# Kernel tuning notes

Measured on AMD Instinct MI355X. Metric: run time of the kernel, lower is better.

Reference implementation:

```python
import jax, jax.numpy as jnp
import numpy as np

H = 16          # query heads
KV = 8          # kv heads
D = 256         # head_dim
HID = 3584      # hidden_size
ROPE_BASE = 10000.0
SCALING = 256.0 ** -0.5          # query_pre_attn_scalar ** -0.5
SOFTCAP = 50.0                   # attn_logit_softcapping
WINDOW = 1536 - 1                # sliding_window - 1 (layer_idx 0 is even)


def _rope_neox(x, positions):
    # x: [T, nh, D]; neox style: rotate the two halves of the head dim
    half = D // 2
    inv_freq = 1.0 / (ROPE_BASE ** (jnp.arange(0, D, 2, dtype=jnp.float32) / D))  # [half]
    freqs = positions.astype(jnp.float32)[:, None] * inv_freq[None, :]            # [T, half]
    cos = jnp.cos(freqs)[:, None, :]  # [T, 1, half]
    sin = jnp.sin(freqs)[:, None, :]
    x1, x2 = x[..., :half], x[..., half:]
    return jnp.concatenate([x1 * cos - x2 * sin, x2 * cos + x1 * sin], axis=-1)


def setup_inputs() -> dict:
    key = jax.random.key(0)
    k1, k2, k3 = jax.random.split(key, 3)
    T = 3072
    hidden_states = jax.random.normal(k1, (T, HID), dtype=jnp.float32)
    w_qkv = jax.random.normal(k2, (H * D + 2 * KV * D, HID), dtype=jnp.float32) * 0.02
    w_o = jax.random.normal(k3, (HID, H * D), dtype=jnp.float32) * 0.02
    positions = jnp.arange(T, dtype=jnp.int64)
    return {"positions": positions, "hidden_states": hidden_states,
            "w_qkv": w_qkv, "w_o": w_o}


def reference(positions, hidden_states, w_qkv, w_o):
    T = hidden_states.shape[0]
    qkv = hidden_states @ w_qkv.T                       # [T, (H+2KV)*D]
    q, k, v = jnp.split(qkv, [H * D, H * D + KV * D], axis=-1)
    q = q.reshape(T, H, D)
    k = k.reshape(T, KV, D)
    v = v.reshape(T, KV, D)
    q = _rope_neox(q, positions)
    k = _rope_neox(k, positions)
    # GQA: repeat kv heads (2 query heads per kv head)
    k = jnp.repeat(k, H // KV, axis=1)                  # [T, H, D]
    v = jnp.repeat(v, H // KV, axis=1)
    scores = jnp.einsum('thd,shd->hts', q, k) * SCALING  # [H, T, T]
    scores = SOFTCAP * jnp.tanh(scores / SOFTCAP)       # logit softcapping
    i = positions[:, None]
    j = positions[None, :]
    mask = (j <= i) & (i - j <= WINDOW)                 # causal + sliding window
    scores = jnp.where(mask[None, :, :], scores, -jnp.inf)
    probs = jax.nn.softmax(scores, axis=-1)
    attn = jnp.einsum('hts,shd->thd', probs, v).reshape(T, H * D)
    return attn @ w_o.T                                 # [T, HID]
```

## Files before the change

kernel.cpp:

```cpp
#include <hip/hip_runtime.h>
#include <math.h>

typedef unsigned short u16;
typedef __attribute__((ext_vector_type(8))) short short8;
typedef __attribute__((ext_vector_type(4))) float f32x4;
typedef __attribute__((ext_vector_type(4))) unsigned short u16x4;

#define HN 16
#define KVH 8
#define DH 256
#define HID 3584
#define T_LEN 3072
#define QKV_N 8192
#define O_N 4096
#define WIN 1535
#define SCALING 0.0625f
#define SOFTCAP 50.0f
#define KOFF 4096
#define VOFF 6144
#define PSTR 72
#define NJT 48
#define M_FIX 20.0f

__device__ __forceinline__ u16 f2bf(float f) {
  unsigned u = __float_as_uint(f);
  u += 0x7FFFu + ((u >> 16) & 1u);
  return (u16)(u >> 16);
}
__device__ __forceinline__ float bf2f(u16 b) {
  return __uint_as_float(((unsigned)b) << 16);
}

__device__ __forceinline__ void gload_lds16(const void* g, void* l) {
  __builtin_amdgcn_global_load_lds(
      (const __attribute__((address_space(1))) void*)g,
      (__attribute__((address_space(3))) void*)l, 16, 0, 0);
}

__device__ __forceinline__ f32x4 mfma_bf16(short8 a, short8 b, f32x4 c) {
  return __builtin_amdgcn_mfma_f32_16x16x32_bf16(a, b, c, 0, 0, 0);
}

#define BARX()                                  \
  do {                                          \
    __builtin_amdgcn_sched_barrier(0);          \
    __builtin_amdgcn_s_barrier();               \
    __builtin_amdgcn_sched_barrier(0);          \
  } while (0)

__global__ __launch_bounds__(256) void cvt2_kernel(const float* __restrict__ a,
                                                   u16* __restrict__ da, int nva,
                                                   const float* __restrict__ b,
                                                   u16* __restrict__ db, int nvb,
                                                   float* __restrict__ rtab) {
  const int bid = blockIdx.x;
  if (bid < 1536) {
    int idx = bid * 256 + threadIdx.x;
    int d = idx & 127;
    int t = idx >> 7;
    float inv = exp2f((float)d * (-13.287712379549449f / 128.0f));
    float ang = (float)t * inv;
    float2 cs;
    cs.x = cosf(ang);
    cs.y = sinf(ang);
    *(float2*)(rtab + (size_t)idx * 2) = cs;
  }
  int v = bid * 256 + threadIdx.x;
  const float* src;
  u16* dst;
  if (v < nva) {
    src = a + (size_t)v * 4;
    dst = da + (size_t)v * 4;
  } else if (v < nva + nvb) {
    int u = v - nva;
    src = b + (size_t)u * 4;
    dst = db + (size_t)u * 4;
  } else {
    return;
  }
  float4 x = *(const float4*)src;
  u16x4 o;
  o[0] = f2bf(x.x); o[1] = f2bf(x.y); o[2] = f2bf(x.z); o[3] = f2bf(x.w);
  *(u16x4*)dst = o;
}

template <int OUT_BF16, int ROPE>
__global__ __launch_bounds__(512, 2) void gemm8p(const u16* __restrict__ A,
                                                 const u16* __restrict__ B,
                                                 void* __restrict__ Cv,
                                                 int N, int K, int ntn, int cpx,
                                                 const float* __restrict__ rtab) {
  __shared__ u16 sA[2][256 * 64];
  __shared__ u16 sB[2][256 * 64];

  const int bid = blockIdx.x;
  const int tid = threadIdx.x;
  const int wg = (bid & 7) * cpx + (bid >> 3);
  const int bm = wg / ntn, bn = wg % ntn;
  const int row0 = bm * 256, col0 = bn * 256;
  const int lane = tid & 63, wid = tid >> 6;
  const int wr = wid >> 2, wc = wid & 3;
  const int NT = K >> 6;

  const int srow = lane >> 3;
  const int sg = (lane & 7) ^ srow;

  auto stage = [&](int tau, int kind) {
    if (tau >= NT) return;
    const int b = tau & 1;
    const int rbase = (kind & 1) * 128;
    const u16* src;
    u16* dst;
    if (kind >= 2) {
      src = A + (size_t)(row0 + rbase + wid * 8 + srow) * K + (size_t)tau * 64 + sg * 8;
      dst = &sA[b][(rbase + wid * 8) * 64];
    } else {
      src = B + (size_t)(col0 + rbase + wid * 8 + srow) * K + (size_t)tau * 64 + sg * 8;
      dst = &sB[b][(rbase + wid * 8) * 64];
    }
    gload_lds16(src, dst);
    gload_lds16(src + (size_t)64 * K, dst + 64 * 64);
  };

  f32x4 acc[8][4] = {};
  const int fr = lane & 15;
  const int fh = fr & 7;
  const int gk0 = (lane >> 4) ^ fh;
  const int gk1 = ((lane >> 4) + 4) ^ fh;

  stage(0, 0); stage(0, 1); stage(0, 2); stage(0, 3);
  stage(1, 0); stage(1, 1); stage(1, 2);
  __builtin_amdgcn_sched_barrier(0);
  asm volatile("s_waitcnt vmcnt(6)" ::: "memory");
  BARX();

  for (int u = 0; u < NT; ++u) {
    const int b = u & 1;
    const u16* pA = &sA[b][0];
    const u16* pB = &sB[b][0];
    short8 bf[4][2], afA[2][2], afB[2][2];

#define CMAP(ni) (wc * 32 + ((ni) & 1) * 16 + ((ni) >> 1) * 128)
#define LDB_(ni, kk) (*(const short8*)&pB[(CMAP(ni) + fr) * 64 + (kk ? gk1 : gk0) * 8])
#define LDA_(mi, kk) (*(const short8*)&pA[(wr * 128 + (mi)*16 + fr) * 64 + (kk ? gk1 : gk0) * 8])
#define MFMA2(AF, mi0)                                                   \
  __builtin_amdgcn_s_setprio(1);                                        \
  _Pragma("unroll") for (int ni = 0; ni < 4; ++ni) {                    \
    acc[mi0][ni] = mfma_bf16(AF[0][0], bf[ni][0], acc[mi0][ni]);        \
    acc[mi0][ni] = mfma_bf16(AF[0][1], bf[ni][1], acc[mi0][ni]);        \
    acc[mi0 + 1][ni] = mfma_bf16(AF[1][0], bf[ni][0], acc[mi0 + 1][ni]);\
    acc[mi0 + 1][ni] = mfma_bf16(AF[1][1], bf[ni][1], acc[mi0 + 1][ni]);\
  }                                                                      \
  __builtin_amdgcn_s_setprio(0);                                        \
  asm volatile("s_waitcnt lgkmcnt(0)" ::: "memory");

#pragma unroll
    for (int ni = 0; ni < 4; ++ni) { bf[ni][0] = LDB_(ni, 0); bf[ni][1] = LDB_(ni, 1); }
    afA[0][0] = LDA_(0, 0); afA[0][1] = LDA_(0, 1);
    afA[1][0] = LDA_(1, 0); afA[1][1] = LDA_(1, 1);
    stage(u + 1, 3);
    BARX();
    MFMA2(afA, 0);
    BARX();
    afA[0][0] = LDA_(2, 0); afA[0][1] = LDA_(2, 1);
    afA[1][0] = LDA_(3, 0); afA[1][1] = LDA_(3, 1);
    stage(u + 2, 0);
    BARX();
    MFMA2(afA, 2);
    BARX();
    afA[0][0] = LDA_(4, 0); afA[0][1] = LDA_(4, 1);
    afA[1][0] = LDA_(5, 0); afA[1][1] = LDA_(5, 1);
    afB[0][0] = LDA_(6, 0); afB[0][1] = LDA_(6, 1);
    afB[1][0] = LDA_(7, 0); afB[1][1] = LDA_(7, 1);
    stage(u + 2, 1);
    BARX();
    MFMA2(afA, 4);
    BARX();
    stage(u + 2, 2);
    __builtin_amdgcn_sched_barrier(0);
    if (u + 2 < NT) {
      asm volatile("s_waitcnt vmcnt(6)" ::: "memory");
    } else {
      asm volatile("s_waitcnt vmcnt(0)" ::: "memory");
    }
    BARX();
    MFMA2(afB, 6);
    BARX();
#undef LDB_
#undef LDA_
#undef MFMA2
  }

  if (ROPE && bn < 24) {
#pragma unroll
    for (int mi = 0; mi < 8; ++mi) {
#pragma unroll
      for (int nh = 0; nh < 2; ++nh) {
        const int dlo = wc * 32 + nh * 16 + fr;
#pragma unroll
        for (int j = 0; j < 4; ++j) {
          const int r = row0 + wr * 128 + mi * 16 + (lane >> 4) * 4 + j;
          float2 cs = *(const float2*)(rtab + ((size_t)(r << 7) + dlo) * 2);
          float xlo = acc[mi][nh][j];
          float xhi = acc[mi][nh + 2][j];
          ((u16*)Cv)[(size_t)r * N + col0 + dlo] = f2bf(xlo * cs.x - xhi * cs.y);
          ((u16*)Cv)[(size_t)r * N + col0 + dlo + 128] = f2bf(xhi * cs.x + xlo * cs.y);
        }
      }
    }
  } else {
#pragma unroll
    for (int mi = 0; mi < 8; ++mi) {
#pragma unroll
      for (int ni = 0; ni < 4; ++ni) {
        const int r = row0 + wr * 128 + mi * 16 + (lane >> 4) * 4;
        const int c = col0 + CMAP(ni) + fr;
#pragma unroll
        for (int j = 0; j < 4; ++j) {
          float v = acc[mi][ni][j];
          if (OUT_BF16)
            ((u16*)Cv)[(size_t)(r + j) * N + c] = f2bf(v);
          else
            ((float*)Cv)[(size_t)(r + j) * N + c] = v;
        }
      }
    }
  }
#undef CMAP
}

__global__ __launch_bounds__(256) void vtrans_kernel(const u16* __restrict__ qkv,
                                                     u16* __restrict__ vt) {
  __shared__ u16 tile[256 * 72];
  const int jb = blockIdx.x * 64;
  const int kvh = blockIdx.y;
  const int tid = threadIdx.x;
  const int t = tid & 63, dc = tid >> 6;

  const u16* src = qkv + (size_t)(jb + t) * QKV_N + VOFF + kvh * DH + dc * 64;
#pragma unroll
  for (int i = 0; i < 8; ++i) {
    short8 v = *(const short8*)(src + i * 8);
    int d0 = dc * 64 + i * 8;
#pragma unroll
    for (int j = 0; j < 8; ++j) tile[(d0 + j) * 72 + t] = (u16)(short)v[j];
  }
  __syncthreads();

  u16* dst = vt + ((size_t)kvh * NJT + blockIdx.x) * 16384;
#pragma unroll
  for (int s = 0; s < 8; ++s) {
    int G = s * 256 + tid;
    int d = G >> 3, g = G & 7;
    short8 x = *(const short8*)&tile[d * 72 + ((g ^ (d & 7)) * 8)];
    *(short8*)(dst + G * 8) = x;
  }
}

__global__ __launch_bounds__(256) void attn_kernel(const u16* __restrict__ qkv,
                                                   const u16* __restrict__ vt,
                                                   u16* __restrict__ po,
                                                   float* __restrict__ ml) {
  const int wg = blockIdx.x;
  const int kvh = wg & 7;
  const int rest = wg >> 3;
  const int qt = rest >> 2;
  const int c = (rest >> 1) & 1;
  const int h = kvh * 2 + (rest & 1);
  const int qb = qt * 64;
  const int tid = threadIdx.x, lane = tid & 63, w = tid >> 6;

  __shared__ u16 sK[64 * 256];
  __shared__ u16 sVt[64 * 256];
  __shared__ u16 sP[4][16 * PSTR];

  int jmin = qb - WIN; if (jmin < 0) jmin = 0;
  const int jt0 = jmin >> 6, jt1 = qb >> 6;
  const int nt = jt1 - jt0 + 1;
  const int half = (nt + 1) >> 1;
  const int t_beg = (c == 0) ? jt0 : jt0 + half;
  const int t_end = (c == 0) ? jt0 + half : jt1 + 1;

  const int qrow = qb + w * 16 + (lane & 15);
  short8 qf[8];
  {
    const u16* qp = qkv + (size_t)qrow * QKV_N + h * DH + (lane >> 4) * 8;
#pragma unroll
    for (int kc = 0; kc < 8; ++kc) qf[kc] = *(const short8*)(qp + kc * 32);
  }

  f32x4 O[16];
#pragma unroll
  for (int i = 0; i < 16; ++i) O[i] = f32x4{0.f, 0.f, 0.f, 0.f};
  float lrow[4] = {0.f, 0.f, 0.f, 0.f};

  const int dl = lane & 15;
  const int vb0 = dl * 64 + (((lane >> 4)) ^ (dl & 7)) * 8;
  const int vb1 = dl * 64 + (((lane >> 4) + 4) ^ (dl & 7)) * 8;

  for (int jt = t_beg; jt < t_end; ++jt) {
    const int jb = jt * 64;
#pragma unroll
    for (int i = 0; i < 8; ++i) {
      int rl = w * 16 + i * 2 + (lane >> 5);
      int g = (lane & 31) ^ (rl & 7);
      gload_lds16(qkv + (size_t)(jb + rl) * QKV_N + KOFF + kvh * DH + g * 8,
                  &sK[(w * 16 + i * 2) * 256]);
    }
    {
      const u16* vtile = vt + ((size_t)kvh * NJT + jt) * 16384;
#pragma unroll
      for (int s = 0; s < 8; ++s) {
        int id = w * 8 + s;
        gload_lds16(vtile + id * 512 + lane * 8, &sVt[id * 512]);
      }
    }
    __syncthreads();

    f32x4 S[4];
#pragma unroll
    for (int nf = 0; nf < 4; ++nf) S[nf] = f32x4{0.f, 0.f, 0.f, 0.f};
#pragma unroll
    for (int nf = 0; nf < 4; ++nf) {
      int krow = nf * 16 + (lane & 15);
#pragma unroll
      for (int kc = 0; kc < 8; ++kc) {
        int g = (kc * 4 + (lane >> 4)) ^ (krow & 7);
        short8 kf = *(const short8*)&sK[krow * 256 + g * 8];
        S[nf] = mfma_bf16(qf[kc], kf, S[nf]);
      }
    }

#pragma unroll
    for (int r = 0; r < 4; ++r) {
      const int irow = qb + w * 16 + (lane >> 4) * 4 + r;
      const int ql = (lane >> 4) * 4 + r;
#pragma unroll
      for (int nf = 0; nf < 4; ++nf) {
        int j = jb + nf * 16 + (lane & 15);
        float x = S[nf][r] * (SCALING / SOFTCAP);
        float e2 = __expf(-2.0f * fabsf(x));
        float th = (1.0f - e2) / (1.0f + e2);
        th = x >= 0.0f ? th : -th;
        float val = SOFTCAP * th;
        bool ok = (j <= irow) && (irow - j <= WIN);
        float p = ok ? __expf(val - M_FIX) : 0.0f;
        lrow[r] += p;
        sP[w][ql * PSTR + nf * 16 + (lane & 15)] = f2bf(p);
      }
    }

    short8 pf0 = *(const short8*)&sP[w][(lane & 15) * PSTR + (lane >> 4) * 8];
    short8 pf1 = *(const short8*)&sP[w][(lane & 15) * PSTR + 32 + (lane >> 4) * 8];
#pragma unroll
    for (int nf = 0; nf < 16; ++nf) {
      short8 vf0 = *(const short8*)&sVt[nf * 1024 + vb0];
      short8 vf1 = *(const short8*)&sVt[nf * 1024 + vb1];
      O[nf] = mfma_bf16(pf0, vf0, O[nf]);
      O[nf] = mfma_bf16(pf1, vf1, O[nf]);
    }
    __syncthreads();
  }

#pragma unroll
  for (int r = 0; r < 4; ++r) {
#pragma unroll
    for (int off = 8; off >= 1; off >>= 1) lrow[r] += __shfl_xor(lrow[r], off);
  }

#pragma unroll
  for (int nf = 0; nf < 16; ++nf) {
    int d = nf * 16 + (lane & 15);
#pragma unroll
    for (int r = 0; r < 4; ++r) {
      int trow = qb + w * 16 + (lane >> 4) * 4 + r;
      po[(((size_t)c * T_LEN + trow) * HN + h) * DH + d] = f2bf(O[nf][r]);
    }
  }
  if ((lane & 15) == 0) {
#pragma unroll
    for (int r = 0; r < 4; ++r) {
      int trow = qb + w * 16 + (lane >> 4) * 4 + r;
      size_t mi = (((size_t)c * T_LEN + trow) * HN + h) * 2;
      ml[mi] = M_FIX;
      ml[mi + 1] = lrow[r];
    }
  }
}

__global__ __launch_bounds__(256) void combine_kernel(const u16* __restrict__ po,
                                                      const float* __restrict__ ml,
                                                      u16* __restrict__ attnb,
                                                      const float* __restrict__ wo,
                                                      u16* __restrict__ wob) {
  const int t = blockIdx.x;
  const int h = threadIdx.x >> 4;
  const int d0 = (threadIdx.x & 15) * 16;
  const size_t row = (size_t)t * HN + h;
  const float l0 = ml[row * 2 + 1];
  const float l1 = ml[(size_t)T_LEN * HN * 2 + row * 2 + 1];
  const float inv = 1.0f / (l0 + l1);
  const size_t i0 = row * DH + d0;
  const size_t i1 = (size_t)T_LEN * HN * DH + i0;
#pragma unroll
  for (int half = 0; half < 2; ++half) {
    short8 x0 = *(const short8*)(po + i0 + half * 8);
    short8 x1 = *(const short8*)(po + i1 + half * 8);
    short8 o;
#pragma unroll
    for (int j = 0; j < 8; ++j)
      o[j] = (short)f2bf((bf2f((u16)x0[j]) + bf2f((u16)x1[j])) * inv);
    *(short8*)(attnb + i0 + half * 8) = o;
  }

  const int nv = (HID * O_N) / 4;
  for (int v = blockIdx.x * 256 + threadIdx.x; v < nv; v += T_LEN * 256) {
    float4 x = *(const float4*)(wo + (size_t)v * 4);
    u16x4 o;
    o[0] = f2bf(x.x); o[1] = f2bf(x.y); o[2] = f2bf(x.z); o[3] = f2bf(x.w);
    *(u16x4*)(wob + (size_t)v * 4) = o;
  }
}

extern "C" void kernel_launch(void* const* d_in, const int* in_sizes, int n_in,
                              void* d_out, int out_size, void* d_ws, size_t ws_size,
                              hipStream_t stream) {
  const float* hidden = (const float*)d_in[1];
  const float* w_qkv = (const float*)d_in[2];
  const float* w_o = (const float*)d_in[3];
  float* out = (float*)d_out;
  char* ws = (char*)d_ws;

  u16* wqkvb = (u16*)(ws);
  u16* po = (u16*)(ws);
  float* ml = (float*)(ws + 50331648);
  u16* attnb = (u16*)(ws);
  u16* hb = (u16*)(ws + 58720256);
  u16* vtb = (u16*)(ws + 58720256);
  u16* qkvb = (u16*)(ws + 80740352);
  u16* wob = (u16*)(ws + 80740352);
  float* ropetab = out;

  {
    int nva = T_LEN * HID / 4;
    int nvb = QKV_N * HID / 4;
    cvt2_kernel<<<dim3((nva + nvb + 255) / 256), 256, 0, stream>>>(
        hidden, hb, nva, w_qkv, wqkvb, nvb, ropetab);
  }
  gemm8p<1, 1><<<dim3(384), 512, 0, stream>>>(hb, wqkvb, qkvb, QKV_N, HID, 32, 48,
                                              ropetab);
  vtrans_kernel<<<dim3(NJT, KVH), 256, 0, stream>>>(qkvb, vtb);
  attn_kernel<<<dim3(1536), 256, 0, stream>>>(qkvb, vtb, po, ml);
  combine_kernel<<<dim3(T_LEN), 256, 0, stream>>>(po, ml, attnb, w_o, wob);
  gemm8p<0, 0><<<dim3(168), 512, 0, stream>>>(attnb, wob, out, HID, O_N, 14, 21,
                                              nullptr);
}
```

Measured before the change: 537.5 us.

## Split tail M-tiles of QKV GEMM into half-height blocks to balance waves

Replaces the templated QKV GEMM launch with a dedicated kernel whose first 256 blocks compute full 256x256 tiles and whose remaining 256 blocks compute 128x256 half tiles for the last third of rows. This is meant to remove the wave-quantization tail where half the CUs idle in the second round. The half-tile path has lower arithmetic intensity per staged B tile and adds code size. The output GEMM is simplified to a float-only non-template kernel.

```diff
diff --git a/kernel.cpp b/kernel.cpp
--- a/kernel.cpp
+++ b/kernel.cpp
@@ -84,12 +84,202 @@
   *(u16x4*)dst = o;
 }
 
-template <int OUT_BF16, int ROPE>
+__global__ __launch_bounds__(512, 2) void gemm1_kernel(const u16* __restrict__ A,
+                                                       const u16* __restrict__ B,
+                                                       u16* __restrict__ C,
+                                                       const float* __restrict__ rtab) {
+  __shared__ u16 sA[2][256 * 64];
+  __shared__ u16 sB[2][256 * 64];
+
+  const int N = QKV_N, K = HID;
+  const int bid = blockIdx.x;
+  const int tid = threadIdx.x;
+  const int lane = tid & 63, wid = tid >> 6;
+  const int NT = K >> 6;
+  const int srow = lane >> 3;
+  const int sg = (lane & 7) ^ srow;
+  const int fr = lane & 15;
+  const int fh = fr & 7;
+  const int gk0 = (lane >> 4) ^ fh;
+  const int gk1 = ((lane >> 4) + 4) ^ fh;
+
+  int bm, bn, row0, mhalf = 0;
+  const int isFull = (bid < 256);
+  if (isFull) {
+    const int wg = (bid & 7) * 32 + (bid >> 3);
+    bm = wg >> 5; bn = wg & 31;
+    row0 = bm * 256;
+  } else {
+    const int j = bid - 256;
+    mhalf = j >> 7;
+    const int j2 = j & 127;
+    const int s = (j2 & 7) * 16 + (j2 >> 3);
+    bm = 8 + (s >> 5); bn = s & 31;
+    row0 = bm * 256 + mhalf * 128;
+  }
+  const int col0 = bn * 256;
+  const int wc = wid & 3;
+
+  auto stage = [&](int tau, int kind) {
+    if (tau >= NT) return;
+    const int b = tau & 1;
+    const u16* src;
+    u16* dst;
+    if (kind >= 2) {
+      const int rbase = (kind - 2) * 128;
+      src = A + (size_t)(row0 + rbase + wid * 8 + srow) * K + (size_t)tau * 64 + sg * 8;
+      dst = &sA[b][(rbase + wid * 8) * 64];
+    } else {
+      const int rbase = kind * 128;
+      src = B + (size_t)(col0 + rbase + wid * 8 + srow) * K + (size_t)tau * 64 + sg * 8;
+      dst = &sB[b][(rbase + wid * 8) * 64];
+    }
+    gload_lds16(src, dst);
+    gload_lds16(src + (size_t)64 * K, dst + 64 * 64);
+  };
+
+#define CMAP(ni) (wc * 32 + ((ni) & 1) * 16 + ((ni) >> 1) * 128)
+#define LDB_(pB, ni, kk) (*(const short8*)&pB[(CMAP(ni) + fr) * 64 + (kk ? gk1 : gk0) * 8])
+#define LDA_(pA, mrow, kk) (*(const short8*)&pA[((mrow) + fr) * 64 + (kk ? gk1 : gk0) * 8])
+#define MFMA2(AF, acc0, acc1)                                            \
+  __builtin_amdgcn_s_setprio(1);                                        \
+  _Pragma("unroll") for (int ni = 0; ni < 4; ++ni) {                    \
+    acc0[ni] = mfma_bf16(AF[0][0], bf[ni][0], acc0[ni]);                \
+    acc0[ni] = mfma_bf16(AF[0][1], bf[ni][1], acc0[ni]);                \
+    acc1[ni] = mfma_bf16(AF[1][0], bf[ni][0], acc1[ni]);                \
+    acc1[ni] = mfma_bf16(AF[1][1], bf[ni][1], acc1[ni]);                \
+  }                                                                      \
+  __builtin_amdgcn_s_setprio(0);                                        \
+  asm volatile("s_waitcnt lgkmcnt(0)" ::: "memory");
+
+#define ROPE_WRITE(ACC, MROWG)                                           \
+  _Pragma("unroll") for (int nh = 0; nh < 2; ++nh) {                    \
+    const int dlo = wc * 32 + nh * 16 + fr;                             \
+    _Pragma("unroll") for (int j = 0; j < 4; ++j) {                     \
+      const int r = (MROWG) + (lane >> 4) * 4 + j;                      \
+      float2 cs = *(const float2*)(rtab + ((size_t)(r << 7) + dlo) * 2);\
+      float xlo = ACC[nh][j], xhi = ACC[nh + 2][j];                     \
+      C[(size_t)r * N + col0 + dlo] = f2bf(xlo * cs.x - xhi * cs.y);    \
+      C[(size_t)r * N + col0 + dlo + 128] = f2bf(xhi * cs.x + xlo * cs.y); \
+    }                                                                    \
+  }
+#define PLAIN_WRITE(ACC, MROWG)                                          \
+  _Pragma("unroll") for (int ni = 0; ni < 4; ++ni) {                    \
+    const int r0 = (MROWG) + (lane >> 4) * 4;                           \
+    const int c = col0 + CMAP(ni) + fr;                                 \
+    _Pragma("unroll") for (int j = 0; j < 4; ++j)                       \
+      C[(size_t)(r0 + j) * N + c] = f2bf(ACC[ni][j]);                   \
+  }
+
+  if (isFull) {
+    const int wr = wid >> 2;
+    f32x4 acc[8][4] = {};
+    stage(0, 0); stage(0, 1); stage(0, 2); stage(0, 3);
+    stage(1, 0); stage(1, 1); stage(1, 2);
+    __builtin_amdgcn_sched_barrier(0);
+    asm volatile("s_waitcnt vmcnt(6)" ::: "memory");
+    BARX();
+
+    for (int u = 0; u < NT; ++u) {
+      const int b = u & 1;
+      const u16* pA = &sA[b][0];
+      const u16* pB = &sB[b][0];
+      short8 bf[4][2], afA[2][2], afB[2][2];
+#pragma unroll
+      for (int ni = 0; ni < 4; ++ni) { bf[ni][0] = LDB_(pB, ni, 0); bf[ni][1] = LDB_(pB, ni, 1); }
+      afA[0][0] = LDA_(pA, wr * 128 + 0 * 16, 0); afA[0][1] = LDA_(pA, wr * 128 + 0 * 16, 1);
+      afA[1][0] = LDA_(pA, wr * 128 + 1 * 16, 0); afA[1][1] = LDA_(pA, wr * 128 + 1 * 16, 1);
+      stage(u + 1, 3);
+      BARX();
+      MFMA2(afA, acc[0], acc[1]);
+      BARX();
+      afA[0][0] = LDA_(pA, wr * 128 + 2 * 16, 0); afA[0][1] = LDA_(pA, wr * 128 + 2 * 16, 1);
+      afA[1][0] = LDA_(pA, wr * 128 + 3 * 16, 0); afA[1][1] = LDA_(pA, wr * 128 + 3 * 16, 1);
+      stage(u + 2, 0);
+      BARX();
+      MFMA2(afA, acc[2], acc[3]);
+      BARX();
+      afA[0][0] = LDA_(pA, wr * 128 + 4 * 16, 0); afA[0][1] = LDA_(pA, wr * 128 + 4 * 16, 1);
+      afA[1][0] = LDA_(pA, wr * 128 + 5 * 16, 0); afA[1][1] = LDA_(pA, wr * 128 + 5 * 16, 1);
+      afB[0][0] = LDA_(pA, wr * 128 + 6 * 16, 0); afB[0][1] = LDA_(pA, wr * 128 + 6 * 16, 1);
+      afB[1][0] = LDA_(pA, wr * 128 + 7 * 16, 0); afB[1][1] = LDA_(pA, wr * 128 + 7 * 16, 1);
+      stage(u + 2, 1);
+      BARX();
+      MFMA2(afA, acc[4], acc[5]);
+      BARX();
+      stage(u + 2, 2);
+      __builtin_amdgcn_sched_barrier(0);
+      if (u + 2 < NT) {
+        asm volatile("s_waitcnt vmcnt(6)" ::: "memory");
+      } else {
+        asm volatile("s_waitcnt vmcnt(0)" ::: "memory");
+      }
+      BARX();
+      MFMA2(afB, acc[6], acc[7]);
+      BARX();
+    }
+    if (bn < 24) {
+#pragma unroll
+      for (int mi = 0; mi < 8; ++mi) { ROPE_WRITE(acc[mi], row0 + wr * 128 + mi * 16); }
+    } else {
+#pragma unroll
+      for (int mi = 0; mi < 8; ++mi) { PLAIN_WRITE(acc[mi], row0 + wr * 128 + mi * 16); }
+    }
+  } else {
+    const int wr = wid >> 2;
+    f32x4 acc[4][4] = {};
+    stage(0, 0); stage(0, 1); stage(0, 2);
+    stage(1, 0); stage(1, 1);
+    __builtin_amdgcn_sched_barrier(0);
+    asm volatile("s_waitcnt vmcnt(4)" ::: "memory");
+    BARX();
+
+    for (int u = 0; u < NT; ++u) {
+      const int b = u & 1;
+      const u16* pA = &sA[b][0];
+      const u16* pB = &sB[b][0];
+      short8 bf[4][2], afA[2][2], afB[2][2];
+#pragma unroll
+      for (int ni = 0; ni < 4; ++ni) { bf[ni][0] = LDB_(pB, ni, 0); bf[ni][1] = LDB_(pB, ni, 1); }
+      afA[0][0] = LDA_(pA, wr * 64 + 0 * 16, 0); afA[0][1] = LDA_(pA, wr * 64 + 0 * 16, 1);
+      afA[1][0] = LDA_(pA, wr * 64 + 1 * 16, 0); afA[1][1] = LDA_(pA, wr * 64 + 1 * 16, 1);
+      stage(u + 1, 2);
+      BARX();
+      MFMA2(afA, acc[0], acc[1]);
+      BARX();
+      afB[0][0] = LDA_(pA, wr * 64 + 2 * 16, 0); afB[0][1] = LDA_(pA, wr * 64 + 2 * 16, 1);
+      afB[1][0] = LDA_(pA, wr * 64 + 3 * 16, 0); afB[1][1] = LDA_(pA, wr * 64 + 3 * 16, 1);
+      stage(u + 2, 0); stage(u + 2, 1);
+      __builtin_amdgcn_sched_barrier(0);
+      if (u + 2 < NT) {
+        asm volatile("s_waitcnt vmcnt(4)" ::: "memory");
+      } else {
+        asm volatile("s_waitcnt vmcnt(0)" ::: "memory");
+      }
+      BARX();
+      MFMA2(afB, acc[2], acc[3]);
+      BARX();
+    }
+    if (bn < 24) {
+#pragma unroll
+      for (int mi = 0; mi < 4; ++mi) { ROPE_WRITE(acc[mi], row0 + wr * 64 + mi * 16); }
+    } else {
+#pragma unroll
+      for (int mi = 0; mi < 4; ++mi) { PLAIN_WRITE(acc[mi], row0 + wr * 64 + mi * 16); }
+    }
+  }
+#undef CMAP
+#undef LDB_
+#undef LDA_
+#undef MFMA2
+#undef ROPE_WRITE
+#undef PLAIN_WRITE
+}
+
 __global__ __launch_bounds__(512, 2) void gemm8p(const u16* __restrict__ A,
                                                  const u16* __restrict__ B,
-                                                 void* __restrict__ Cv,
-                                                 int N, int K, int ntn, int cpx,
-                                                 const float* __restrict__ rtab) {
+                                                 float* __restrict__ C,
+                                                 int N, int K, int ntn, int cpx) {
   __shared__ u16 sA[2][256 * 64];
   __shared__ u16 sB[2][256 * 64];
 
@@ -186,47 +376,23 @@
     BARX();
     MFMA2(afB, 6);
     BARX();
+#undef CMAP
 #undef LDB_
 #undef LDA_
 #undef MFMA2
   }
 
-  if (ROPE && bn < 24) {
-#pragma unroll
-    for (int mi = 0; mi < 8; ++mi) {
-#pragma unroll
-      for (int nh = 0; nh < 2; ++nh) {
-        const int dlo = wc * 32 + nh * 16 + fr;
-#pragma unroll
-        for (int j = 0; j < 4; ++j) {
-          const int r = row0 + wr * 128 + mi * 16 + (lane >> 4) * 4 + j;
-          float2 cs = *(const float2*)(rtab + ((size_t)(r << 7) + dlo) * 2);
-          float xlo = acc[mi][nh][j];
-          float xhi = acc[mi][nh + 2][j];
-          ((u16*)Cv)[(size_t)r * N + col0 + dlo] = f2bf(xlo * cs.x - xhi * cs.y);
-          ((u16*)Cv)[(size_t)r * N + col0 + dlo + 128] = f2bf(xhi * cs.x + xlo * cs.y);
-        }
-      }
-    }
-  } else {
-#pragma unroll
-    for (int mi = 0; mi < 8; ++mi) {
-#pragma unroll
-      for (int ni = 0; ni < 4; ++ni) {
-        const int r = row0 + wr * 128 + mi * 16 + (lane >> 4) * 4;
-        const int c = col0 + CMAP(ni) + fr;
-#pragma unroll
-        for (int j = 0; j < 4; ++j) {
-          float v = acc[mi][ni][j];
-          if (OUT_BF16)
-            ((u16*)Cv)[(size_t)(r + j) * N + c] = f2bf(v);
-          else
-            ((float*)Cv)[(size_t)(r + j) * N + c] = v;
-        }
-      }
-    }
-  }
-#undef CMAP
+#pragma unroll
+  for (int mi = 0; mi < 8; ++mi) {
+#pragma unroll
+    for (int ni = 0; ni < 4; ++ni) {
+      const int r = row0 + wr * 128 + mi * 16 + (lane >> 4) * 4;
+      const int c = col0 + wc * 32 + (ni & 1) * 16 + (ni >> 1) * 128 + fr;
+#pragma unroll
+      for (int j = 0; j < 4; ++j)
+        C[(size_t)(r + j) * N + c] = acc[mi][ni][j];
+    }
+  }
 }
 
 __global__ __launch_bounds__(256) void vtrans_kernel(const u16* __restrict__ qkv,
@@ -447,11 +613,9 @@
     cvt2_kernel<<<dim3((nva + nvb + 255) / 256), 256, 0, stream>>>(
         hidden, hb, nva, w_qkv, wqkvb, nvb, ropetab);
   }
-  gemm8p<1, 1><<<dim3(384), 512, 0, stream>>>(hb, wqkvb, qkvb, QKV_N, HID, 32, 48,
-                                              ropetab);
+  gemm1_kernel<<<dim3(512), 512, 0, stream>>>(hb, wqkvb, qkvb, ropetab);
   vtrans_kernel<<<dim3(NJT, KVH), 256, 0, stream>>>(qkvb, vtb);
   attn_kernel<<<dim3(1536), 256, 0, stream>>>(qkvb, vtb, po, ml);
   combine_kernel<<<dim3(T_LEN), 256, 0, stream>>>(po, ml, attnb, w_o, wob);
-  gemm8p<0, 0><<<dim3(168), 512, 0, stream>>>(attnb, wob, out, HID, O_N, 14, 21,
-                                              nullptr);
-}
+  gemm8p<<<dim3(168), 512, 0, stream>>>(attnb, wob, out, HID, O_N, 14, 21);
+}
```

Result: no change. 541.0 us (+0.6%).
